# Performance work log

Measured on AMD Instinct MI355X. Metric: run time of the kernel, lower is better.

## Reference

```python
import jax, jax.numpy as jnp
import numpy as np

T, H, I, E, K = 1024, 2048, 1024, 16, 2

def setup_inputs() -> dict:
    key = jax.random.key(0)
    ks = jax.random.split(key, 6)
    return {
        "hidden_states": jax.random.normal(ks[0], (T, H), jnp.float32),
        "gate_w": jax.random.normal(ks[1], (E, H), jnp.float32) * 0.02,
        "bias": jax.random.normal(ks[2], (E,), jnp.float32) * 0.01,
        "w1": jax.random.normal(ks[3], (E, H, I), jnp.float32) * 0.02,
        "w3": jax.random.normal(ks[4], (E, H, I), jnp.float32) * 0.02,
        "w2": jax.random.normal(ks[5], (E, I, H), jnp.float32) * 0.02,
    }

def reference(hidden_states, gate_w, bias, w1, w3, w2):
    x = hidden_states  # [T, H]
    # Router gating linear in fp32 (gate.weight cast to float32 in source)
    logits = x.astype(jnp.float32) @ gate_w.T            # [T, E]
    scores = jax.nn.softmax(logits, axis=-1)             # scoring_func='softmax'
    # grouped_topk with num_expert_group=topk_group=1 == plain top-k;
    # e_score_correction_bias only biases expert *selection*.
    _, topk_idx = jax.lax.top_k(scores + bias[None, :], K)   # [T, K]
    topk_w = jnp.take_along_axis(scores, topk_idx, axis=1)   # weights from raw scores
    topk_w = topk_w / jnp.sum(topk_w, axis=-1, keepdims=True)  # renormalize=True
    # Scatter top-k weights into dense combine matrix [T, E]
    rows = jnp.arange(T)[:, None]
    combine = jnp.zeros((T, E), jnp.float32).at[rows, topk_idx].add(topk_w)
    # SwiGLU experts computed densely over all experts, masked by combine
    h1 = jnp.einsum('th,ehi->eti', x, w1)                # [E, T, I]
    h3 = jnp.einsum('th,ehi->eti', x, w3)
    he = jax.nn.silu(h1) * h3
    ye = jnp.einsum('eti,eih->eth', he, w2)              # [E, T, H]
    out = jnp.einsum('eth,te->th', ye, combine.astype(x.dtype))  # weighted combine
    return out
```

## Files before the change

kernel.cpp:

```cpp
#include <hip/hip_runtime.h>
#include <stdint.h>

#define Ttok 1024
#define Hdim 2048
#define Idim 1024
#define Enum 16
#define NKH  64
#define NKO  32

typedef __attribute__((ext_vector_type(8))) short  short8;
typedef __attribute__((ext_vector_type(4))) float  f32x4;

__device__ __forceinline__ unsigned short f2bf(float f) {
    union { float f; uint32_t u; } v; v.f = f;
    uint32_t u = v.u;
    return (unsigned short)((u + 0x7FFFu + ((u >> 16) & 1u)) >> 16);
}
__device__ __forceinline__ uint32_t cvtpk(float lo, float hi) {
    uint32_t d;
    asm("v_cvt_pk_bf16_f32 %0, %1, %2" : "=v"(d) : "v"(lo), "v"(hi));
    return d;
}
__device__ __forceinline__ void gld_lds16(const void* g, void* l) {
    __builtin_amdgcn_global_load_lds(
        (const __attribute__((address_space(1))) unsigned int*)g,
        (__attribute__((address_space(3))) unsigned int*)l, 16, 0, 0);
}

__global__ __launch_bounds__(256) void k_router(
    const float* __restrict__ x, const float* __restrict__ gw,
    const float* __restrict__ bias,
    int* __restrict__ counts, int* __restrict__ tids, float* __restrict__ tws)
{
    __shared__ __align__(16) float xrow[Hdim];
    __shared__ float lg[Enum];
    const int t = blockIdx.x;
    const float* xr = x + (size_t)t * Hdim;

    for (int i = threadIdx.x; i < Hdim / 4; i += 256)
        ((f32x4*)xrow)[i] = ((const f32x4*)xr)[i];
    __syncthreads();

    const int lane = threadIdx.x & 63;
    const int wid  = threadIdx.x >> 6;
    for (int e = wid; e < Enum; e += 4) {
        const float* g = gw + (size_t)e * Hdim;
        float s = 0.f;
        for (int j = lane; j < Hdim; j += 64) s += xrow[j] * g[j];
        #pragma unroll
        for (int off = 32; off; off >>= 1) s += __shfl_xor(s, off);
        if (lane == 0) lg[e] = s;
    }
    __syncthreads();

    if (threadIdx.x == 0) {
        float m = lg[0];
        #pragma unroll
        for (int e = 1; e < Enum; ++e) m = fmaxf(m, lg[e]);
        float sc[Enum]; float sum = 0.f;
        #pragma unroll
        for (int e = 0; e < Enum; ++e) { float ex = expf(lg[e] - m); sc[e] = ex; sum += ex; }
        float inv = 1.f / sum;
        #pragma unroll
        for (int e = 0; e < Enum; ++e) sc[e] *= inv;
        int i0 = 0; float b0 = sc[0] + bias[0];
        #pragma unroll
        for (int e = 1; e < Enum; ++e) { float bb = sc[e] + bias[e]; if (bb > b0) { b0 = bb; i0 = e; } }
        int i1 = -1; float b1 = -1e30f;
        #pragma unroll
        for (int e = 0; e < Enum; ++e) {
            if (e == i0) continue;
            float bb = sc[e] + bias[e]; if (bb > b1) { b1 = bb; i1 = e; }
        }
        float w0 = sc[i0], w1v = sc[i1];
        float winv = 1.f / (w0 + w1v);
        w0 *= winv; w1v *= winv;
        int p0 = atomicAdd(&counts[i0], 1);
        tids[i0 * Ttok + p0] = t; tws[i0 * Ttok + p0] = w0;
        int p1 = atomicAdd(&counts[i1], 1);
        tids[i1 * Ttok + p1] = t; tws[i1 * Ttok + p1] = w1v;
    }
}

__global__ __launch_bounds__(256) void k_gather(
    const float* __restrict__ x, const int* __restrict__ counts,
    const int* __restrict__ tids, unsigned short* __restrict__ Xg)
{
    const int e = blockIdx.y >> 2, c = blockIdx.y & 3;
    const int Ne = counts[e];
    const int s  = blockIdx.x;
    const int r  = threadIdx.x & 63;
    const int kq = threadIdx.x >> 6;
    const int row = c * 64 + r;
    const bool valid = row < Ne;
    const int tok = valid ? tids[e * Ttok + row] : 0;
    const float* xr = x + (size_t)tok * Hdim;

    #pragma unroll
    for (int j = 0; j < 8; ++j) {
        int kg = s * 32 + j * 4 + kq;
        uint4 o = make_uint4(0, 0, 0, 0);
        if (valid) {
            f32x4 p0 = *(const f32x4*)(xr + kg * 8);
            f32x4 p1 = *(const f32x4*)(xr + kg * 8 + 4);
            o.x = cvtpk(p0[0], p0[1]); o.y = cvtpk(p0[2], p0[3]);
            o.z = cvtpk(p1[0], p1[1]); o.w = cvtpk(p1[2], p1[3]);
        }
        *(uint4*)(Xg + ((size_t)(e * 256 + kg) * 256 + row) * 8) = o;
    }
}

__global__ __launch_bounds__(512, 2) void k_h(
    const unsigned short* __restrict__ Xg,
    const float* __restrict__ w1, const float* __restrict__ w3,
    unsigned short* __restrict__ He)
{
    const int e    = blockIdx.y;
    const int cb   = blockIdx.x;
    const int col0 = cb * 64;
    const int tid  = threadIdx.x;
    const int lane = tid & 63;
    const int wid  = tid >> 6;
    const int l15  = lane & 15;
    const int kq   = lane >> 4;
    const int wr   = wid >> 2, wc = wid & 3;

    __shared__ float          Wr[4][32][128];
    __shared__ unsigned short Ar[4][4][256][8];

    const unsigned short* asrc[2]; int aoff[2];
    #pragma unroll
    for (int qq = 0; qq < 2; ++qq) {
        int q = wid * 2 + qq;
        asrc[qq] = Xg + ((size_t)(e * 256 + (q >> 2)) * 256 + (q & 3) * 64 + lane) * 8;
        aoff[qq] = q * 1024;
    }
    const float* wsrcp[2]; int woff[2];
    #pragma unroll
    for (int pp = 0; pp < 2; ++pp) {
        int p  = wid * 2 + pp;
        int kr = p * 2 + (lane >> 5);
        int lc = lane & 31;
        wsrcp[pp] = (lc < 16)
            ? (w1 + ((size_t)e * Hdim + kr) * Idim + col0 + lc * 4)
            : (w3 + ((size_t)e * Hdim + kr) * Idim + col0 + (lc - 16) * 4);
        woff[pp] = p * 1024;
    }

    f32x4 acc1[8], acc3[8];
    #pragma unroll
    for (int a = 0; a < 8; ++a) { acc1[a] = (f32x4)(0.f); acc3[a] = (f32x4)(0.f); }

    char* ArB = (char*)&Ar[0][0][0][0];
    char* WrB = (char*)&Wr[0][0][0];

    auto ISSUE = [&](int s, int buf) {
        #pragma unroll
        for (int qq = 0; qq < 2; ++qq)
            gld_lds16(asrc[qq] + (size_t)s * 8192, ArB + buf * 16384 + aoff[qq]);
        #pragma unroll
        for (int pp = 0; pp < 2; ++pp)
            gld_lds16(wsrcp[pp] + (size_t)s * 32 * Idim, WrB + buf * 16384 + woff[pp]);
    };
    auto CONSUME = [&](int ri) {
        float b1f[8], b3f[8];
        #pragma unroll
        for (int j = 0; j < 8; ++j) {
            b1f[j] = Wr[ri][kq * 8 + j][wc * 16 + l15];
            b3f[j] = Wr[ri][kq * 8 + j][64 + wc * 16 + l15];
        }
        short8 b1, b3;
        uint32_t* b1u = (uint32_t*)&b1; uint32_t* b3u = (uint32_t*)&b3;
        #pragma unroll
        for (int j = 0; j < 4; ++j) {
            b1u[j] = cvtpk(b1f[2 * j], b1f[2 * j + 1]);
            b3u[j] = cvtpk(b3f[2 * j], b3f[2 * j + 1]);
        }
        #pragma unroll
        for (int fr = 0; fr < 8; ++fr) {
            short8 a = *(const short8*)&Ar[ri][kq][wr * 128 + fr * 16 + l15][0];
            acc1[fr] = __builtin_amdgcn_mfma_f32_16x16x32_bf16(a, b1, acc1[fr], 0, 0, 0);
            acc3[fr] = __builtin_amdgcn_mfma_f32_16x16x32_bf16(a, b3, acc3[fr], 0, 0, 0);
        }
    };
    auto STEP = [&](int s, int ri) {
        int s2 = s + 2 < NKH ? s + 2 : NKH - 1;
        ISSUE(s2, (ri + 2) & 3);
        asm volatile("s_waitcnt vmcnt(8)" ::: "memory");
        __builtin_amdgcn_s_barrier();
        CONSUME(ri);
    };

    ISSUE(0, 0); ISSUE(1, 1);
    for (int i = 0; i < NKH; i += 4) {
        STEP(i, 0); STEP(i + 1, 1); STEP(i + 2, 2); STEP(i + 3, 3);
    }
    asm volatile("s_waitcnt vmcnt(0)" ::: "memory");

    const int colh = col0 + wc * 16 + l15;
    unsigned short* Hc = He + ((size_t)(e * 128 + (colh >> 3)) * 256) * 8 + (colh & 7);
    #pragma unroll
    for (int fr = 0; fr < 8; ++fr) {
        int rbase = wr * 128 + fr * 16 + kq * 4;
        #pragma unroll
        for (int k = 0; k < 4; ++k) {
            float h1 = acc1[fr][k], h3 = acc3[fr][k];
            float he = h1 * h3 * __builtin_amdgcn_rcpf(1.f + __expf(-h1));
            Hc[(size_t)(rbase + k) * 8] = f2bf(he);
        }
    }
}

__global__ __launch_bounds__(512, 2) void k_o(
    const unsigned short* __restrict__ He,
    const float* __restrict__ w2,
    const int* __restrict__ counts, const int* __restrict__ tids,
    const float* __restrict__ tws,
    float* __restrict__ out)
{
    const int e    = blockIdx.y;
    const int Ne   = counts[e];
    const int col0 = blockIdx.x * 128;
    const int tid  = threadIdx.x;
    const int lane = tid & 63;
    const int wid  = tid >> 6;
    const int l15  = lane & 15;
    const int kq   = lane >> 4;
    const int wr   = wid >> 2, wc = wid & 3;

    __shared__ float          Wr[4][32][128];
    __shared__ unsigned short Ar[4][4][256][8];

    const unsigned short* asrc[2]; int aoff[2];
    #pragma unroll
    for (int qq = 0; qq < 2; ++qq) {
        int q = wid * 2 + qq;
        asrc[qq] = He + ((size_t)(e * 128 + (q >> 2)) * 256 + (q & 3) * 64 + lane) * 8;
        aoff[qq] = q * 1024;
    }
    const float* wsrcp[2]; int woff[2];
    #pragma unroll
    for (int pp = 0; pp < 2; ++pp) {
        int p  = wid * 2 + pp;
        int kr = p * 2 + (lane >> 5);
        int lc = lane & 31;
        wsrcp[pp] = w2 + ((size_t)e * Idim + kr) * Hdim + col0 + lc * 4;
        woff[pp] = p * 1024;
    }

    f32x4 acc[8][2];
    #pragma unroll
    for (int a = 0; a < 8; ++a) { acc[a][0] = (f32x4)(0.f); acc[a][1] = (f32x4)(0.f); }

    char* ArB = (char*)&Ar[0][0][0][0];
    char* WrB = (char*)&Wr[0][0][0];

    auto ISSUE = [&](int s, int buf) {
        #pragma unroll
        for (int qq = 0; qq < 2; ++qq)
            gld_lds16(asrc[qq] + (size_t)s * 8192, ArB + buf * 16384 + aoff[qq]);
        #pragma unroll
        for (int pp = 0; pp < 2; ++pp)
            gld_lds16(wsrcp[pp] + (size_t)s * 32 * Hdim, WrB + buf * 16384 + woff[pp]);
    };
    auto CONSUME = [&](int ri) {
        float bf[2][8];
        #pragma unroll
        for (int fc = 0; fc < 2; ++fc)
            #pragma unroll
            for (int j = 0; j < 8; ++j)
                bf[fc][j] = Wr[ri][kq * 8 + j][wc * 32 + fc * 16 + l15];
        short8 b[2];
        #pragma unroll
        for (int fc = 0; fc < 2; ++fc) {
            uint32_t* bu = (uint32_t*)&b[fc];
            #pragma unroll
            for (int j = 0; j < 4; ++j)
                bu[j] = cvtpk(bf[fc][2 * j], bf[fc][2 * j + 1]);
        }
        #pragma unroll
        for (int fr = 0; fr < 8; ++fr) {
            short8 a = *(const short8*)&Ar[ri][kq][wr * 128 + fr * 16 + l15][0];
            acc[fr][0] = __builtin_amdgcn_mfma_f32_16x16x32_bf16(a, b[0], acc[fr][0], 0, 0, 0);
            acc[fr][1] = __builtin_amdgcn_mfma_f32_16x16x32_bf16(a, b[1], acc[fr][1], 0, 0, 0);
        }
    };
    auto STEP = [&](int s, int ri) {
        int s2 = s + 2 < NKO ? s + 2 : NKO - 1;
        ISSUE(s2, (ri + 2) & 3);
        asm volatile("s_waitcnt vmcnt(8)" ::: "memory");
        __builtin_amdgcn_s_barrier();
        CONSUME(ri);
    };

    ISSUE(0, 0); ISSUE(1, 1);
    for (int i = 0; i < NKO; i += 4) {
        STEP(i, 0); STEP(i + 1, 1); STEP(i + 2, 2); STEP(i + 3, 3);
    }
    asm volatile("s_waitcnt vmcnt(0)" ::: "memory");

    #pragma unroll
    for (int fr = 0; fr < 8; ++fr) {
        #pragma unroll
        for (int k = 0; k < 4; ++k) {
            int grow = wr * 128 + fr * 16 + kq * 4 + k;
            if (grow < Ne) {
                int   tk = tids[e * Ttok + grow];
                float w  = tws[e * Ttok + grow];
                #pragma unroll
                for (int fc = 0; fc < 2; ++fc)
                    atomicAdd(&out[(size_t)tk * Hdim + col0 + wc * 32 + fc * 16 + l15],
                              w * acc[fr][fc][k]);
            }
        }
    }
}

extern "C" void kernel_launch(void* const* d_in, const int* in_sizes, int n_in,
                              void* d_out, int out_size, void* d_ws, size_t ws_size,
                              hipStream_t stream)
{
    const float* x    = (const float*)d_in[0];
    const float* gw   = (const float*)d_in[1];
    const float* bias = (const float*)d_in[2];
    const float* w1   = (const float*)d_in[3];
    const float* w3   = (const float*)d_in[4];
    const float* w2   = (const float*)d_in[5];
    float* out = (float*)d_out;

    char* ws = (char*)d_ws;
    int*            counts = (int*)ws;
    int*            tids   = (int*)(ws + 1024);
    float*          tws    = (float*)(ws + 66560);
    unsigned short* Xg     = (unsigned short*)(ws + 132096);
    unsigned short* He     = (unsigned short*)(ws + 16909312);

    hipMemsetAsync(counts, 0, Enum * sizeof(int), stream);
    hipMemsetAsync(out, 0, (size_t)Ttok * Hdim * sizeof(float), stream);

    k_router<<<dim3(Ttok), dim3(256), 0, stream>>>(x, gw, bias, counts, tids, tws);
    k_gather<<<dim3(8, 64), dim3(256), 0, stream>>>(x, counts, tids, Xg);
    k_h<<<dim3(16, Enum), dim3(512), 0, stream>>>(Xg, w1, w3, He);
    k_o<<<dim3(16, Enum), dim3(512), 0, stream>>>(He, w2, counts, tids, tws, out);
}
```

Before: 216.3 us.

## Deepen LDS prefetch to three stages and rotate weight columns against bank conflicts

Both expert GEMM kernels now keep three K-stages in flight instead of two. The issue-ahead load is placed after the barrier, so the single barrier also guards reuse of the 4-slot ring buffer. The fp32 weight tile is written to LDS with a 16-column rotation on alternating row groups, and readers apply a matching shift by kq, to reduce LDS bank conflicts on the transposed B reads. Launch bounds drop the min-blocks hint from 2 to 1, which lets the compiler use more registers at the possible cost of occupancy.

```diff
diff --git a/kernel.cpp b/kernel.cpp
--- a/kernel.cpp
+++ b/kernel.cpp
@@ -110,7 +110,7 @@
     }
 }
 
-__global__ __launch_bounds__(512, 2) void k_h(
+__global__ __launch_bounds__(512, 1) void k_h(
     const unsigned short* __restrict__ Xg,
     const float* __restrict__ w1, const float* __restrict__ w3,
     unsigned short* __restrict__ He)
@@ -138,12 +138,13 @@
     const float* wsrcp[2]; int woff[2];
     #pragma unroll
     for (int pp = 0; pp < 2; ++pp) {
-        int p  = wid * 2 + pp;
-        int kr = p * 2 + (lane >> 5);
-        int lc = lane & 31;
-        wsrcp[pp] = (lc < 16)
-            ? (w1 + ((size_t)e * Hdim + kr) * Idim + col0 + lc * 4)
-            : (w3 + ((size_t)e * Hdim + kr) * Idim + col0 + (lc - 16) * 4);
+        int p     = wid * 2 + pp;
+        int kr    = p * 2 + (lane >> 5);
+        int shift = ((p >> 2) & 1) * 16;
+        int cg    = (((lane & 31) * 4) + 128 - shift) & 127;
+        wsrcp[pp] = (cg < 64)
+            ? (w1 + ((size_t)e * Hdim + kr) * Idim + col0 + cg)
+            : (w3 + ((size_t)e * Hdim + kr) * Idim + col0 + (cg - 64));
         woff[pp] = p * 1024;
     }
 
@@ -163,11 +164,12 @@
             gld_lds16(wsrcp[pp] + (size_t)s * 32 * Idim, WrB + buf * 16384 + woff[pp]);
     };
     auto CONSUME = [&](int ri) {
+        const int sh = (kq & 1) * 16;
         float b1f[8], b3f[8];
         #pragma unroll
         for (int j = 0; j < 8; ++j) {
-            b1f[j] = Wr[ri][kq * 8 + j][wc * 16 + l15];
-            b3f[j] = Wr[ri][kq * 8 + j][64 + wc * 16 + l15];
+            b1f[j] = Wr[ri][kq * 8 + j][(wc * 16 + l15 + sh) & 127];
+            b3f[j] = Wr[ri][kq * 8 + j][(64 + wc * 16 + l15 + sh) & 127];
         }
         short8 b1, b3;
         uint32_t* b1u = (uint32_t*)&b1; uint32_t* b3u = (uint32_t*)&b3;
@@ -183,17 +185,14 @@
             acc3[fr] = __builtin_amdgcn_mfma_f32_16x16x32_bf16(a, b3, acc3[fr], 0, 0, 0);
         }
     };
-    auto STEP = [&](int s, int ri) {
-        int s2 = s + 2 < NKH ? s + 2 : NKH - 1;
-        ISSUE(s2, (ri + 2) & 3);
+
+    ISSUE(0, 0); ISSUE(1, 1); ISSUE(2, 2);
+    for (int s = 0; s < NKH; ++s) {
         asm volatile("s_waitcnt vmcnt(8)" ::: "memory");
         __builtin_amdgcn_s_barrier();
-        CONSUME(ri);
-    };
-
-    ISSUE(0, 0); ISSUE(1, 1);
-    for (int i = 0; i < NKH; i += 4) {
-        STEP(i, 0); STEP(i + 1, 1); STEP(i + 2, 2); STEP(i + 3, 3);
+        int sn = s + 3 < NKH ? s + 3 : NKH - 1;
+        ISSUE(sn, (s + 3) & 3);
+        CONSUME(s & 3);
     }
     asm volatile("s_waitcnt vmcnt(0)" ::: "memory");
 
@@ -211,7 +210,7 @@
     }
 }
 
-__global__ __launch_bounds__(512, 2) void k_o(
+__global__ __launch_bounds__(512, 1) void k_o(
     const unsigned short* __restrict__ He,
     const float* __restrict__ w2,
     const int* __restrict__ counts, const int* __restrict__ tids,
@@ -241,11 +240,12 @@
     const float* wsrcp[2]; int woff[2];
     #pragma unroll
     for (int pp = 0; pp < 2; ++pp) {
-        int p  = wid * 2 + pp;
-        int kr = p * 2 + (lane >> 5);
-        int lc = lane & 31;
-        wsrcp[pp] = w2 + ((size_t)e * Idim + kr) * Hdim + col0 + lc * 4;
-        woff[pp] = p * 1024;
+        int p     = wid * 2 + pp;
+        int kr    = p * 2 + (lane >> 5);
+        int shift = ((p >> 2) & 1) * 16;
+        int cg    = (((lane & 31) * 4) + 128 - shift) & 127;
+        wsrcp[pp] = w2 + ((size_t)e * Idim + kr) * Hdim + col0 + cg;
+        woff[pp]  = p * 1024;
     }
 
     f32x4 acc[8][2];
@@ -264,12 +264,13 @@
             gld_lds16(wsrcp[pp] + (size_t)s * 32 * Hdim, WrB + buf * 16384 + woff[pp]);
     };
     auto CONSUME = [&](int ri) {
+        const int sh = (kq & 1) * 16;
         float bf[2][8];
         #pragma unroll
         for (int fc = 0; fc < 2; ++fc)
             #pragma unroll
             for (int j = 0; j < 8; ++j)
-                bf[fc][j] = Wr[ri][kq * 8 + j][wc * 32 + fc * 16 + l15];
+                bf[fc][j] = Wr[ri][kq * 8 + j][(wc * 32 + fc * 16 + l15 + sh) & 127];
         short8 b[2];
         #pragma unroll
         for (int fc = 0; fc < 2; ++fc) {
@@ -285,17 +286,14 @@
             acc[fr][1] = __builtin_amdgcn_mfma_f32_16x16x32_bf16(a, b[1], acc[fr][1], 0, 0, 0);
         }
     };
-    auto STEP = [&](int s, int ri) {
-        int s2 = s + 2 < NKO ? s + 2 : NKO - 1;
-        ISSUE(s2, (ri + 2) & 3);
+
+    ISSUE(0, 0); ISSUE(1, 1); ISSUE(2, 2);
+    for (int s = 0; s < NKO; ++s) {
         asm volatile("s_waitcnt vmcnt(8)" ::: "memory");
         __builtin_amdgcn_s_barrier();
-        CONSUME(ri);
-    };
-
-    ISSUE(0, 0); ISSUE(1, 1);
-    for (int i = 0; i < NKO; i += 4) {
-        STEP(i, 0); STEP(i + 1, 1); STEP(i + 2, 2); STEP(i + 3, 3);
+        int sn = s + 3 < NKO ? s + 3 : NKO - 1;
+        ISSUE(sn, (s + 3) & 3);
+        CONSUME(s & 3);
     }
     asm volatile("s_waitcnt vmcnt(0)" ::: "memory");
 
```

Measured after the change: 271.2 us. +25.4%, slower.
